# Performance work log

Measured on AMD Instinct MI355X. Metric: run time of the kernel, lower is better.

Reference implementation:

```python
import jax, jax.numpy as jnp
import numpy as np

P = 30          # points per cloud (nr_points)
K = 20          # knn neighbors (k)
KS = 5          # spline kernel size (control points)
FN = 10         # filter_nr
EPS = 1e-8


def setup_inputs() -> dict:
    key = jax.random.key(0)
    ks = jax.random.split(key, 7)
    B = 16384
    pos = jax.random.normal(ks[0], (B * P, 3), dtype=jnp.float32)
    W = jax.random.normal(ks[1], (KS, FN), dtype=jnp.float32) * 0.5
    b_dsc = jnp.zeros((FN,), dtype=jnp.float32)
    w1 = jax.random.normal(ks[2], (FN, 256), dtype=jnp.float32) * (1.0 / np.sqrt(FN))
    b1 = jnp.zeros((256,), dtype=jnp.float32)
    w2 = jax.random.normal(ks[3], (256, 40), dtype=jnp.float32) * (1.0 / np.sqrt(256.0))
    b2 = jnp.zeros((40,), dtype=jnp.float32)
    return {"pos": pos, "W": W, "b_dsc": b_dsc, "w1": w1, "b1": b1, "w2": w2, "b2": b2}


def _dsc(pos, W, b_dsc):
    # pos: [N,3] -> per-point directional spline conv features [N, FN]
    B = pos.shape[0] // P
    p = pos.reshape(B, P, 3)
    # knn within each cloud (loop=False): pairwise sq dists, mask self
    d2 = jnp.sum((p[:, :, None, :] - p[:, None, :, :]) ** 2, axis=-1)  # [B,P,P]
    d2 = d2 + jnp.eye(P, dtype=d2.dtype) * 1e10
    _, idx = jax.lax.top_k(-d2, K)  # [B,P,K] nearest neighbor indices
    nb = jax.vmap(lambda pts, ii: pts[ii])(p, idx)  # [B,P,K,3] gather
    rel = nb - p[:, :, None, :]                      # [B,P,K,3]
    # normalize neighborhood into unit ball
    norm = jnp.sqrt(jnp.sum(rel * rel, axis=-1) + EPS)      # [B,P,K]
    scale = jnp.max(norm, axis=-1, keepdims=True) + EPS     # [B,P,1]
    rel_n = rel / scale[..., None]
    # dominant local direction via power iteration on 3x3 covariance
    C = jnp.einsum('bpki,bpkj->bpij', rel_n, rel_n)  # [B,P,3,3]
    v = jnp.ones((B, P, 3), dtype=pos.dtype) / jnp.sqrt(3.0)
    for _ in range(8):
        v = jnp.einsum('bpij,bpj->bpi', C, v)
        v = v / (jnp.sqrt(jnp.sum(v * v, axis=-1, keepdims=True)) + EPS)
    # directional coordinate in [-1,1] -> spline parameter in [0, KS-1]
    t = jnp.einsum('bpki,bpi->bpk', rel_n, v)        # [B,P,K]
    u = jnp.clip((t + 1.0) * 0.5, 0.0, 1.0) * (KS - 1)
    i0 = jnp.clip(jnp.floor(u), 0, KS - 2).astype(jnp.int32)  # [B,P,K]
    frac = (u - i0.astype(u.dtype))[..., None]                 # [B,P,K,1]
    feat = W[i0] * (1.0 - frac) + W[i0 + 1] * frac             # [B,P,K,FN]
    y = jnp.mean(feat, axis=2) + b_dsc                         # [B,P,FN]
    return y.reshape(B * P, FN)


def reference(pos, W, b_dsc, w1, b1, w2, b2):
    y = _dsc(pos, W, b_dsc)                  # [N, FN]
    y = jax.nn.sigmoid(y)
    ys = y.reshape(-1, P, FN).mean(axis=1)   # [B, FN]
    h = jax.nn.elu(ys @ w1 + b1)             # [B, 256]
    logits = h @ w2 + b2                     # [B, 40]
    return jax.nn.log_softmax(logits, axis=1)
```

## Files before the change

kernel.cpp:

```cpp
#include <hip/hip_runtime.h>
#include <math.h>

#define NP 30
#define KNN 20
#define KS 5
#define FN 10
#define EPS 1e-8f
#define CPB 8
#define T1 256

typedef __attribute__((ext_vector_type(8))) short short8v;
typedef __attribute__((ext_vector_type(4))) float float4v;

__device__ __forceinline__ float satf(float x) {
    return fminf(fmaxf(x, 0.0f), 1.0f);
}
__device__ __forceinline__ unsigned short bf16r(float f) {
    unsigned u = __float_as_uint(f);
    u += 0x7fffu + ((u >> 16) & 1u);
    return (unsigned short)(u >> 16);
}
__device__ __forceinline__ int hA_idx(int row, int col ) {
    return row * 256 + ((((col >> 3) ^ (row & 7)) << 3) | (col & 7));
}

__global__ __launch_bounds__(T1, 7) void fused_kernel(
    const float* __restrict__ pos,
    const float* __restrict__ W,
    const float* __restrict__ b_dsc,
    const float* __restrict__ w1,
    const float* __restrict__ b1,
    const float* __restrict__ w2,
    const float* __restrict__ b2,
    float* __restrict__ out,
    int B)
{
    __shared__ float4 ptsF[CPB * NP];
    __shared__ float sbuf[CPB * NP][FN + 1];
    __shared__ float wS[KS * FN];
    __shared__ float bS[FN];
    __shared__ float ysS[CPB][FN];
    __shared__ __align__(16) unsigned short hA[16 * 256];
    __shared__ float Lg[CPB][48];

    const int tid  = threadIdx.x;
    const int base = blockIdx.x * CPB;
    const int w    = tid >> 6;
    const int lane = tid & 63;

    {
        const int lim = min(CPB * NP * 3, B * NP * 3 - base * NP * 3);
        for (int d = tid; d < lim; d += T1) {
            float v  = pos[(size_t)base * (NP * 3) + d];
            int   pt = d / 3;
            ((float*)&ptsF[pt])[d - pt * 3] = v;
        }
    }
    if (tid < KS * FN) wS[tid] = W[tid];
    if (tid < FN)      bS[tid] = b_dsc[tid];
    __syncthreads();

    const int c = tid / NP;
    const int i = tid - c * NP;
    const bool active = (tid < CPB * NP) && (base + c < B);

    if (active) {
        const float4* cp = &ptsF[c * NP];
        const float4 own = cp[i];
        const float ox = own.x, oy = own.y, oz = own.z;

        float vals[32];
        #pragma unroll
        for (int j = 0; j < NP; ++j) {
            float4 q = cp[j];
            float dx = q.x - ox, dy = q.y - oy, dz = q.z - oz;
            vals[j] = fmaf(dz, dz, fmaf(dy, dy, dx * dx));
            if ((j % 5) == 4) asm volatile("" ::: "memory");
        }
        vals[30] = 1e11f;
        vals[31] = 1e11f;

        #pragma unroll
        for (int k = 2; k <= 16; k <<= 1) {
            #pragma unroll
            for (int jj = k >> 1; jj > 0; jj >>= 1) {
                #pragma unroll
                for (int tt = 0; tt < 32; ++tt) {
                    int l = tt ^ jj;
                    if (l > tt) {
                        float a  = vals[tt], b = vals[l];
                        float lo = fminf(a, b), hi = fmaxf(a, b);
                        if ((tt & k) == 0) { vals[tt] = lo; vals[l] = hi; }
                        else               { vals[tt] = hi; vals[l] = lo; }
                    }
                }
            }
        }
        #pragma unroll
        for (int q = 0; q < 16; ++q) vals[16+q] = fmaxf(vals[q], vals[16+q]);
        #pragma unroll
        for (int q = 0; q < 8; ++q)  vals[16+q] = fminf(vals[16+q], vals[24+q]);
        #pragma unroll
        for (int q = 0; q < 4; ++q)  vals[20+q] = fmaxf(vals[16+q], vals[20+q]);
        vals[20] = fminf(vals[20], vals[22]);
        vals[21] = fminf(vals[21], vals[23]);
        const float thr = fminf(vals[20], vals[21]);

        const float scale = sqrtf(thr + EPS) + EPS;
        const float inv_s = __builtin_amdgcn_rcpf(scale);

        asm volatile("" ::: "memory");

        float cxx=0.f, cxy=0.f, cxz=0.f, cyy=0.f, cyz=0.f, czz=0.f;
        #pragma unroll 5
        for (int j = 0; j < NP; ++j) {
            float4 q = cp[j];
            float dx = q.x - ox, dy = q.y - oy, dz = q.z - oz;
            float dd = fmaf(dz, dz, fmaf(dy, dy, dx * dx));
            bool sel = (dd <= thr);
            float mx = sel ? dx : 0.0f;
            float my = sel ? dy : 0.0f;
            float mz = sel ? dz : 0.0f;
            cxx = fmaf(mx, mx, cxx); cxy = fmaf(mx, my, cxy); cxz = fmaf(mx, mz, cxz);
            cyy = fmaf(my, my, cyy); cyz = fmaf(my, mz, cyz); czz = fmaf(mz, mz, czz);
        }

        float tr = cxx + cyy + czz + 1e-30f;
        float rt = __builtin_amdgcn_rcpf(tr);
        float xx = cxx*rt, xy = cxy*rt, xz = cxz*rt;
        float yy = cyy*rt, yz = cyz*rt, zz = czz*rt;
        #pragma unroll
        for (int it = 0; it < 3; ++it) {
            float nxx = fmaf(xx, xx, fmaf(xy, xy, xz * xz));
            float nxy = fmaf(xy, xx + yy, xz * yz);
            float nxz = fmaf(xz, xx + zz, xy * yz);
            float nyy = fmaf(xy, xy, fmaf(yy, yy, yz * yz));
            float nyz = fmaf(yz, yy + zz, xy * xz);
            float nzz = fmaf(xz, xz, fmaf(yz, yz, zz * zz));
            xx = nxx; xy = nxy; xz = nxz; yy = nyy; yz = nyz; zz = nzz;
        }
        float vx = xx + xy + xz;
        float vy = xy + yy + yz;
        float vz = xz + yz + zz;
        float nn = fmaf(vz, vz, fmaf(vy, vy, vx * vx)) + 1e-30f;
        float rr2 = __builtin_amdgcn_rsqf(nn) * inv_s * 2.0f;
        const float wax = vx * rr2, way = vy * rr2, waz = vz * rr2;

        asm volatile("" ::: "memory");

        float a0 = 0.f, a1 = 0.f, a3 = 0.f, s1 = 0.f;
        #pragma unroll 5
        for (int j = 0; j < NP; ++j) {
            float4 q = cp[j];
            float dx = q.x - ox, dy = q.y - oy, dz = q.z - oz;
            float dd = fmaf(dz, dz, fmaf(dy, dy, dx * dx));
            float ur = fmaf(dz, waz, fmaf(dy, way, fmaf(dx, wax, 2.0f)));
            float u  = (dd <= thr) ? ur : 2.0f;
            a0 += satf(1.0f - fabsf(u));
            a1 += satf(1.0f - fabsf(u - 1.0f));
            a3 += satf(1.0f - fabsf(u - 3.0f));
            s1 += u;
        }
        const float P  = 30.0f - a0 - a1 - a3;
        const float Q  = s1 - a1 - 3.0f * a3;
        const float a4 = fmaf(0.5f, Q, -P);
        const float a2 = P - a4 - 10.0f;

        #pragma unroll
        for (int f = 0; f < FN; ++f) {
            float acc = fmaf(a0, wS[0*FN+f],
                        fmaf(a1, wS[1*FN+f],
                        fmaf(a2, wS[2*FN+f],
                        fmaf(a3, wS[3*FN+f],
                             a4 * wS[4*FN+f]))));
            float y = fmaf(acc, 1.0f / (float)KNN, bS[f]);
            sbuf[tid][f] = __builtin_amdgcn_rcpf(1.0f + __expf(-y));
        }
    }
    __syncthreads();

    if (tid < CPB * FN) {
        int c2 = tid / FN;
        int f  = tid - c2 * FN;
        float s = 0.0f;
        #pragma unroll
        for (int jj = 0; jj < NP; ++jj) s += sbuf[c2 * NP + jj][f];
        ysS[c2][f] = (base + c2 < B) ? s * (1.0f / (float)NP) : 0.0f;
    }
    {
        short8v z = {0, 0, 0, 0, 0, 0, 0, 0};
        *(short8v*)&hA[(8 + (tid >> 5)) * 256 + (tid & 31) * 8] = z;
    }
    __syncthreads();

    {
        float wv[FN];
        #pragma unroll
        for (int f = 0; f < FN; ++f) wv[f] = w1[f * 256 + tid];
        float bb = b1[tid];
        #pragma unroll
        for (int cc = 0; cc < CPB; ++cc) {
            float acc = bb;
            #pragma unroll
            for (int f = 0; f < FN; ++f) acc = fmaf(ysS[cc][f], wv[f], acc);
            float h = acc > 0.0f ? acc : __expf(acc) - 1.0f;
            hA[hA_idx(cc, tid)] = bf16r(h);
        }
    }
    __syncthreads();

    if (w < 3) {
        const int  n   = w * 16 + (lane & 15);
        const bool nok = n < 40;
        const int  kg  = (lane >> 4) * 8;
        float4v acc = {0.f, 0.f, 0.f, 0.f};
        #pragma unroll
        for (int s = 0; s < 8; ++s) {
            short8v bfr;
            #pragma unroll
            for (int j = 0; j < 8; ++j) {
                float f = nok ? w2[(s * 32 + kg + j) * 40 + n] : 0.0f;
                bfr[j] = (short)bf16r(f);
            }
            short8v a = *(const short8v*)&hA[hA_idx(lane & 15, kg + s * 32)];
            acc = __builtin_amdgcn_mfma_f32_16x16x32_bf16(a, bfr, acc, 0, 0, 0);
        }
        if (nok) {
            const float bc = b2[n];
            const int   r0 = (lane >> 4) * 4;
            #pragma unroll
            for (int r = 0; r < 4; ++r) {
                int rr = r0 + r;
                if (rr < CPB) Lg[rr][n] = acc[r] + bc;
            }
        }
    }
    __syncthreads();

    if (tid < CPB * 16) {
        int cl = tid >> 4, l = tid & 15;
        float v0 = Lg[cl][l];
        float v1 = Lg[cl][l + 16];
        float v2 = (l < 8) ? Lg[cl][l + 32] : -INFINITY;
        float m = fmaxf(fmaxf(v0, v1), v2);
        #pragma unroll
        for (int msk = 1; msk < 16; msk <<= 1) m = fmaxf(m, __shfl_xor(m, msk));
        float e = __expf(v0 - m) + __expf(v1 - m) + ((l < 8) ? __expf(v2 - m) : 0.0f);
        #pragma unroll
        for (int msk = 1; msk < 16; msk <<= 1) e += __shfl_xor(e, msk);
        float ls = m + __logf(e);
        int cloud = base + cl;
        if (cloud < B) {
            float* op = out + (size_t)cloud * 40;
            op[l]      = v0 - ls;
            op[16 + l] = v1 - ls;
            if (l < 8) op[32 + l] = v2 - ls;
        }
    }
}

extern "C" void kernel_launch(void* const* d_in, const int* in_sizes, int n_in,
                              void* d_out, int out_size, void* d_ws, size_t ws_size,
                              hipStream_t stream) {
    const float* pos   = (const float*)d_in[0];
    const float* W     = (const float*)d_in[1];
    const float* b_dsc = (const float*)d_in[2];
    const float* w1    = (const float*)d_in[3];
    const float* b1    = (const float*)d_in[4];
    const float* w2    = (const float*)d_in[5];
    const float* b2    = (const float*)d_in[6];

    const int N = in_sizes[0] / 3;
    const int B = N / NP;

    const int grid = (B + CPB - 1) / CPB;
    fused_kernel<<<grid, T1, 0, stream>>>(pos, W, b_dsc, w1, b1, w2, b2,
                                          (float*)d_out, B);
}
```

Before: 34.84 us.

## Pack neighbor indices into distance keys and subtract excluded points from covariance

Distances are packed with the point index in their low mantissa bits so the sort also tracks which points fall outside the k nearest. The covariance is accumulated over all points in the first distance loop, and the nine excluded points are then subtracted, removing the second full pass over the cloud. The final merge becomes a half-cleaner plus bitonic sort of the upper half, and the later loop uses an exclusion bitmask instead of recomputing distances. The MLP also reads pooled features through readlane broadcasts instead of shared-memory loads. Truncating mantissa bits and subtracting from the full sum can change tie handling and add rounding error.

```diff
diff --git a/kernel.cpp b/kernel.cpp
--- a/kernel.cpp
+++ b/kernel.cpp
@@ -20,8 +20,14 @@
     u += 0x7fffu + ((u >> 16) & 1u);
     return (unsigned short)(u >> 16);
 }
-__device__ __forceinline__ int hA_idx(int row, int col ) {
+__device__ __forceinline__ float rlanef(float v, int l) {
+    return __int_as_float(__builtin_amdgcn_readlane(__float_as_int(v), l));
+}
+__device__ __forceinline__ int hA_idx(int row, int col) {
     return row * 256 + ((((col >> 3) ^ (row & 7)) << 3) | (col & 7));
+}
+__device__ __forceinline__ float packdi(float d2, int j) {
+    return __uint_as_float((__float_as_uint(d2) & ~31u) | (unsigned)j);
 }
 
 __global__ __launch_bounds__(T1, 7) void fused_kernel(
@@ -39,7 +45,7 @@
     __shared__ float sbuf[CPB * NP][FN + 1];
     __shared__ float wS[KS * FN];
     __shared__ float bS[FN];
-    __shared__ float ysS[CPB][FN];
+    __shared__ float ysS[CPB * FN];
     __shared__ __align__(16) unsigned short hA[16 * 256];
     __shared__ float Lg[CPB][48];
 
@@ -70,15 +76,19 @@
         const float ox = own.x, oy = own.y, oz = own.z;
 
         float vals[32];
+        float cxx=0.f, cxy=0.f, cxz=0.f, cyy=0.f, cyz=0.f, czz=0.f;
         #pragma unroll
         for (int j = 0; j < NP; ++j) {
             float4 q = cp[j];
             float dx = q.x - ox, dy = q.y - oy, dz = q.z - oz;
-            vals[j] = fmaf(dz, dz, fmaf(dy, dy, dx * dx));
+            float d2 = fmaf(dz, dz, fmaf(dy, dy, dx * dx));
+            vals[j] = packdi(d2, j);
+            cxx = fmaf(dx, dx, cxx); cxy = fmaf(dx, dy, cxy); cxz = fmaf(dx, dz, cxz);
+            cyy = fmaf(dy, dy, cyy); cyz = fmaf(dy, dz, cyz); czz = fmaf(dz, dz, czz);
             if ((j % 5) == 4) asm volatile("" ::: "memory");
         }
-        vals[30] = 1e11f;
-        vals[31] = 1e11f;
+        vals[30] = packdi(1e11f, 30);
+        vals[31] = packdi(1e11f, 31);
 
         #pragma unroll
         for (int k = 2; k <= 16; k <<= 1) {
@@ -97,32 +107,35 @@
             }
         }
         #pragma unroll
-        for (int q = 0; q < 16; ++q) vals[16+q] = fmaxf(vals[q], vals[16+q]);
-        #pragma unroll
-        for (int q = 0; q < 8; ++q)  vals[16+q] = fminf(vals[16+q], vals[24+q]);
-        #pragma unroll
-        for (int q = 0; q < 4; ++q)  vals[20+q] = fmaxf(vals[16+q], vals[20+q]);
-        vals[20] = fminf(vals[20], vals[22]);
-        vals[21] = fminf(vals[21], vals[23]);
-        const float thr = fminf(vals[20], vals[21]);
-
-        const float scale = sqrtf(thr + EPS) + EPS;
-        const float inv_s = __builtin_amdgcn_rcpf(scale);
-
-        asm volatile("" ::: "memory");
-
-        float cxx=0.f, cxy=0.f, cxz=0.f, cyy=0.f, cyz=0.f, czz=0.f;
-        #pragma unroll 5
-        for (int j = 0; j < NP; ++j) {
-            float4 q = cp[j];
-            float dx = q.x - ox, dy = q.y - oy, dz = q.z - oz;
-            float dd = fmaf(dz, dz, fmaf(dy, dy, dx * dx));
-            bool sel = (dd <= thr);
-            float mx = sel ? dx : 0.0f;
-            float my = sel ? dy : 0.0f;
-            float mz = sel ? dz : 0.0f;
-            cxx = fmaf(mx, mx, cxx); cxy = fmaf(mx, my, cxy); cxz = fmaf(mx, mz, cxz);
-            cyy = fmaf(my, my, cyy); cyz = fmaf(my, mz, cyz); czz = fmaf(mz, mz, czz);
+        for (int q = 0; q < 16; ++q) {
+            float a = vals[q], b = vals[16 + q];
+            vals[q] = fminf(a, b); vals[16 + q] = fmaxf(a, b);
+        }
+        #pragma unroll
+        for (int jj = 8; jj > 0; jj >>= 1) {
+            #pragma unroll
+            for (int tt = 16; tt < 32; ++tt) {
+                int l = tt ^ jj;
+                if (l > tt) {
+                    float a = vals[tt], b = vals[l];
+                    vals[tt] = fminf(a, b); vals[l] = fmaxf(a, b);
+                }
+            }
+        }
+        const float thr_d2 = __uint_as_float(__float_as_uint(vals[20]) & ~31u);
+        const float scale  = sqrtf(thr_d2 + EPS) + EPS;
+        const float inv_s  = __builtin_amdgcn_rcpf(scale);
+
+        unsigned excl = 0u;
+        #pragma unroll
+        for (int q = 21; q < 30; ++q) {
+            unsigned bq  = __float_as_uint(vals[q]);
+            int      idx = (int)(bq & 31u);
+            float4 p = cp[idx];
+            float dx = p.x - ox, dy = p.y - oy, dz = p.z - oz;
+            cxx = fmaf(-dx, dx, cxx); cxy = fmaf(-dx, dy, cxy); cxz = fmaf(-dx, dz, cxz);
+            cyy = fmaf(-dy, dy, cyy); cyz = fmaf(-dy, dz, cyz); czz = fmaf(-dz, dz, czz);
+            excl |= (1u << idx);
         }
 
         float tr = cxx + cyy + czz + 1e-30f;
@@ -153,9 +166,8 @@
         for (int j = 0; j < NP; ++j) {
             float4 q = cp[j];
             float dx = q.x - ox, dy = q.y - oy, dz = q.z - oz;
-            float dd = fmaf(dz, dz, fmaf(dy, dy, dx * dx));
             float ur = fmaf(dz, waz, fmaf(dy, way, fmaf(dx, wax, 2.0f)));
-            float u  = (dd <= thr) ? ur : 2.0f;
+            float u  = ((excl >> j) & 1u) ? 2.0f : ur;
             a0 += satf(1.0f - fabsf(u));
             a1 += satf(1.0f - fabsf(u - 1.0f));
             a3 += satf(1.0f - fabsf(u - 3.0f));
@@ -185,7 +197,8 @@
         float s = 0.0f;
         #pragma unroll
         for (int jj = 0; jj < NP; ++jj) s += sbuf[c2 * NP + jj][f];
-        ysS[c2][f] = (base + c2 < B) ? s * (1.0f / (float)NP) : 0.0f;
+        ysS[tid] = (base + c2 < B) ? s * (1.0f / (float)NP) : 0.0f;
+        (void)f;
     }
     {
         short8v z = {0, 0, 0, 0, 0, 0, 0, 0};
@@ -194,6 +207,8 @@
     __syncthreads();
 
     {
+        float ya = ysS[lane];
+        float yb = ysS[64 + (lane & 15)];
         float wv[FN];
         #pragma unroll
         for (int f = 0; f < FN; ++f) wv[f] = w1[f * 256 + tid];
@@ -202,7 +217,11 @@
         for (int cc = 0; cc < CPB; ++cc) {
             float acc = bb;
             #pragma unroll
-            for (int f = 0; f < FN; ++f) acc = fmaf(ysS[cc][f], wv[f], acc);
+            for (int f = 0; f < FN; ++f) {
+                const int flat = cc * FN + f;
+                float yv = (flat < 64) ? rlanef(ya, flat) : rlanef(yb, flat - 64);
+                acc = fmaf(yv, wv[f], acc);
+            }
             float h = acc > 0.0f ? acc : __expf(acc) - 1.0f;
             hA[hA_idx(cc, tid)] = bf16r(h);
         }
```

New measurement: 33.37 us. 1.04x faster.
